# Kernel optimization log

Hardware: AMD Instinct MI355X
Metric: run time of the kernel (lower is better)

The kernel has to match this reference:

```python
import jax, jax.numpy as jnp
import numpy as np

B, CIN, H, W = 16, 3, 256, 256
COUT = 64
K = 3          # kernel size
PAD = 1
KK = K * K     # 9 taps
EPS = 1e-5     # BatchNorm eps


def conv3x3(x, w, b=None):
    y = jax.lax.conv_general_dilated(
        x, w, window_strides=(1, 1), padding=[(PAD, PAD), (PAD, PAD)],
        dimension_numbers=("NCHW", "OIHW", "NCHW"))
    if b is not None:
        y = y + b[None, :, None, None]
    return y


def deform_sample(x, off):
    """Bilinear sampling at per-pixel learned offsets (mmcv DeformConv2d, deform_groups=1).
    x: [B,C,H,W], off: [B,2*KK,H,W] interleaved (dy,dx) per kernel tap.
    Returns sampled taps [B,KK,H,W,C]."""
    b, c, h, w = x.shape
    dy = off[:, 0::2]  # [B,KK,H,W]
    dx = off[:, 1::2]
    ky, kx = jnp.meshgrid(jnp.arange(K), jnp.arange(K), indexing="ij")
    ky = (ky.reshape(-1) - PAD).astype(x.dtype)  # tap row offsets: -1,0,1
    kx = (kx.reshape(-1) - PAD).astype(x.dtype)
    gy = jnp.arange(h, dtype=x.dtype)
    gx = jnp.arange(w, dtype=x.dtype)
    # absolute (float) sampling positions per tap
    py = gy[None, None, :, None] + ky[None, :, None, None] + dy  # [B,KK,H,W]
    px = gx[None, None, None, :] + kx[None, :, None, None] + dx
    y0 = jnp.floor(py)
    x0 = jnp.floor(px)
    ly = py - y0
    lx = px - x0
    hy = 1.0 - ly
    hx = 1.0 - lx
    xt = x.transpose(0, 2, 3, 1)  # [B,H,W,C] for channel-last gather
    bi = jnp.arange(b)[:, None, None, None]

    def corner(yi, xi, wgt):
        valid = ((yi >= 0) & (yi <= h - 1) & (xi >= 0) & (xi <= w - 1)).astype(x.dtype)
        yc = jnp.clip(yi, 0, h - 1).astype(jnp.int32)
        xc = jnp.clip(xi, 0, w - 1).astype(jnp.int32)
        return xt[bi, yc, xc] * (wgt * valid)[..., None]  # [B,KK,H,W,C]

    v = (corner(y0, x0, hy * hx)
         + corner(y0, x0 + 1.0, hy * lx)
         + corner(y0 + 1.0, x0, ly * hx)
         + corner(y0 + 1.0, x0 + 1.0, ly * lx))
    return v


def setup_inputs() -> dict:
    key = jax.random.key(0)
    ks = jax.random.split(key, 7)
    x = jax.random.normal(ks[0], (B, CIN, H, W), dtype=jnp.float32)
    # conv_offset: 3x3 conv -> 2*KK offset channels (zero-init in mmcv; use small random)
    w_off = jax.random.normal(ks[1], (2 * KK, CIN, K, K), dtype=jnp.float32) * 0.01
    b_off = jnp.zeros((2 * KK,), dtype=jnp.float32)
    fan = CIN * KK
    w_dcn = jax.random.normal(ks[2], (COUT, CIN, K, K), dtype=jnp.float32) / np.sqrt(fan)
    w_conv = jax.random.normal(ks[3], (COUT, CIN, K, K), dtype=jnp.float32) / np.sqrt(fan)
    b_conv = jax.random.normal(ks[4], (COUT,), dtype=jnp.float32) * 0.01
    gamma = jnp.ones((COUT,), dtype=jnp.float32)
    beta = jnp.zeros((COUT,), dtype=jnp.float32)
    return {"x": x, "w_off": w_off, "b_off": b_off, "w_dcn": w_dcn,
            "w_conv": w_conv, "b_conv": b_conv, "gamma": gamma, "beta": beta}


def reference(x, w_off, b_off, w_dcn, w_conv, b_conv, gamma, beta):
    off = conv3x3(x, w_off, b_off)              # [B,18,H,W]
    taps = deform_sample(x, off)                # [B,KK,H,W,CIN]
    wk = w_dcn.reshape(COUT, CIN, KK).transpose(0, 2, 1)  # [O,KK,C]
    x_dcn = jnp.einsum("bkhwc,okc->bohw", taps, wk)       # deform conv (bias=False)
    x_res = conv3x3(x, w_conv, b_conv)
    y = x_res + x_dcn
    # BatchNorm2d (training mode: batch statistics, biased var)
    mean = y.mean(axis=(0, 2, 3))
    var = y.var(axis=(0, 2, 3))
    yn = (y - mean[None, :, None, None]) * jax.lax.rsqrt(var[None, :, None, None] + EPS)
    yb = yn * gamma[None, :, None, None] + beta[None, :, None, None]
    return yb * jax.nn.sigmoid(yb)  # SiLU
```

## Files before the change

kernel.cpp:

```cpp
#include <hip/hip_runtime.h>
#include <hip/hip_bf16.h>
#include <math.h>

#define BB 16
#define COUTC 64
#define HH 256
#define WWD 256
#define PW 260
#define NBLK (BB*HH)
#define NBLKW (NBLK*4)
#define NPIX (BB*HH*WWD)
#define YTOT ((size_t)NPIX*COUTC)

typedef __attribute__((ext_vector_type(8))) short short8;
typedef __attribute__((ext_vector_type(4))) float f32x4;
typedef __attribute__((ext_vector_type(4))) unsigned short us4;
typedef __attribute__((ext_vector_type(8))) unsigned short us8;

__device__ __forceinline__ unsigned short f2bf(float f) {
    __hip_bfloat16 h = __float2bfloat16(f);
    return __builtin_bit_cast(unsigned short, h);
}
__device__ __forceinline__ float bf2f(unsigned short u) {
    unsigned v = (unsigned)u << 16;
    return __builtin_bit_cast(float, v);
}

__global__ __launch_bounds__(256) void prep_kernel(
    const float* __restrict__ x,
    us4* __restrict__ xp)
{
    const int b  = blockIdx.x / PW;
    const int yr = blockIdx.x % PW - 2;
    const bool rok = (yr >= 0) && (yr < HH);
    const float* xb = x + (size_t)b * (3*HH*WWD) + (size_t)(rok ? yr : 0)*WWD;
    for (int cx = threadIdx.x; cx < PW; cx += 256) {
        const int xx = cx - 2;
        const bool ok = rok && (xx >= 0) && (xx < WWD);
        float f0 = ok ? xb[0*(HH*WWD) + xx] : 0.f;
        float f1 = ok ? xb[1*(HH*WWD) + xx] : 0.f;
        float f2 = ok ? xb[2*(HH*WWD) + xx] : 0.f;
        us4 v = { f2bf(f0), f2bf(f1), f2bf(f2), 0 };
        xp[((size_t)b*PW + (yr+2))*PW + cx] = v;
    }
}

__global__ __launch_bounds__(256) void wtg_kernel(
    const float* __restrict__ w_dcn,
    const float* __restrict__ w_conv,
    const float* __restrict__ w_off,
    unsigned short* __restrict__ wTg,
    unsigned short* __restrict__ wOg)
{
    for (int e = threadIdx.x; e < 512; e += 256) {
        const int kc = e >> 6, n = e & 63;
        const float* wsrc = (kc < 4) ? w_conv : w_dcn;
        const int kb = (kc & 3) * 8;
        us8 v;
        #pragma unroll
        for (int j = 0; j < 8; ++j) {
            int kk = kb + j;
            v[j] = (kk < 27) ? f2bf(wsrc[n*27 + kk]) : (unsigned short)0;
        }
        *(us8*)(wTg + e*8) = v;
    }
    if (threadIdx.x < 128) {
        const int e = threadIdx.x;
        const int nt2 = e >> 6, l = e & 63;
        const int n = nt2*16 + (l & 15);
        const int kb = (l >> 4) * 8;
        us8 v;
        #pragma unroll
        for (int j = 0; j < 8; ++j) {
            int kk = kb + j;
            v[j] = (n < 18 && kk < 27) ? f2bf(w_off[n*27 + kk]) : (unsigned short)0;
        }
        *(us8*)(wOg + e*8) = v;
    }
}

template<bool BF16Y>
__global__ __launch_bounds__(256, 3) void dcn_wave_kernel(
    const float* __restrict__ x,
    const us4* __restrict__ xp,
    const unsigned short* __restrict__ wTg,
    const unsigned short* __restrict__ wOg,
    const float* __restrict__ b_off,
    const float* __restrict__ b_conv,
    float* __restrict__ outf,
    unsigned short* __restrict__ yws,
    float* __restrict__ psum,
    float* __restrict__ psq)
{
    __shared__ __align__(16) char kbuf[32768];
    __shared__ __align__(16) unsigned short sofs[4*64*24];

    const int tid = threadIdx.x;
    const int bid = blockIdx.x;
    const int swz = (bid & 7) * 512 + (bid >> 3);
    const int b = swz >> 8;
    const int h = swz & 255;
    const int w = tid;
    const int l   = tid & 63;
    const int wv  = tid >> 6;
    const int g   = l >> 4;
    const int r15 = l & 15;
    char* kw = kbuf + wv*8192;
    unsigned short* so = sofs + wv*64*24;

    const us4* xpb = xp + (size_t)b*PW*PW;

    us4 xnv[3][3];
    #pragma unroll
    for (int dy = 0; dy < 3; ++dy)
        #pragma unroll
        for (int dx = 0; dx < 3; ++dx)
            xnv[dy][dx] = xpb[(size_t)(h+1+dy)*PW + (w+1+dx)];

    short8 bfr[2][4];
    #pragma unroll
    for (int ks = 0; ks < 2; ++ks)
        #pragma unroll
        for (int nt = 0; nt < 4; ++nt) {
            const int kc = ks*4 + g, n = nt*16 + r15;
            bfr[ks][nt] = *(const short8*)(wTg + (kc*64 + n)*8);
        }
    short8 wof[2];
    #pragma unroll
    for (int nt2 = 0; nt2 < 2; ++nt2)
        wof[nt2] = *(const short8*)(wOg + (nt2*64 + l)*8);

    {
        unsigned short u[32];
        #pragma unroll
        for (int c = 0; c < 3; ++c)
            #pragma unroll
            for (int ky = 0; ky < 3; ++ky)
                #pragma unroll
                for (int kx = 0; kx < 3; ++kx)
                    u[c*9 + ky*3 + kx] = xnv[ky][kx][c];
        #pragma unroll
        for (int k = 27; k < 32; ++k) u[k] = 0;
        #pragma unroll
        for (int c8 = 0; c8 < 4; ++c8) {
            uint4 v;
            v.x = (unsigned)u[c8*8+0] | ((unsigned)u[c8*8+1] << 16);
            v.y = (unsigned)u[c8*8+2] | ((unsigned)u[c8*8+3] << 16);
            v.z = (unsigned)u[c8*8+4] | ((unsigned)u[c8*8+5] << 16);
            v.w = (unsigned)u[c8*8+6] | ((unsigned)u[c8*8+7] << 16);
            *(uint4*)(kw + l*128 + ((c8 ^ (l & 7)) << 4)) = v;
        }
    }

    short8 af0[4];
    #pragma unroll
    for (int mt = 0; mt < 4; ++mt) {
        int row = mt*16 + r15;
        af0[mt] = *(const short8*)(kw + row*128 + ((g ^ (row & 7)) << 4));
    }

    f32x4 dacc[4][2];
    #pragma unroll
    for (int mt = 0; mt < 4; ++mt)
        #pragma unroll
        for (int nt2 = 0; nt2 < 2; ++nt2)
            dacc[mt][nt2] = (f32x4){0.f, 0.f, 0.f, 0.f};
    #pragma unroll
    for (int mt = 0; mt < 4; ++mt)
        #pragma unroll
        for (int nt2 = 0; nt2 < 2; ++nt2)
            dacc[mt][nt2] = __builtin_amdgcn_mfma_f32_16x16x32_bf16(
                af0[mt], wof[nt2], dacc[mt][nt2], 0, 0, 0);

    #pragma unroll
    for (int mt = 0; mt < 4; ++mt)
        #pragma unroll
        for (int nt2 = 0; nt2 < 2; ++nt2) {
            if (nt2 == 1 && r15 >= 2) continue;
            #pragma unroll
            for (int r = 0; r < 4; ++r)
                so[(mt*16 + g*4 + r)*24 + nt2*16 + r15] = f2bf(dacc[mt][nt2][r]);
        }

    float off[18];
    {
        us8 o0 = *(const us8*)(so + l*24);
        us8 o1 = *(const us8*)(so + l*24 + 8);
        us4 o2 = *(const us4*)(so + l*24 + 16);
        #pragma unroll
        for (int j = 0; j < 8; ++j)  off[j]     = bf2f(o0[j]) + b_off[j];
        #pragma unroll
        for (int j = 0; j < 8; ++j)  off[8+j]   = bf2f(o1[j]) + b_off[8+j];
        off[16] = bf2f(o2[0]) + b_off[16];
        off[17] = bf2f(o2[1]) + b_off[17];
    }

    float taps[9][3];
    #pragma unroll
    for (int k = 0; k < 9; ++k) {
        const int ky = k / 3, kx = k % 3;
        float py = (float)(h + ky - 1) + off[2*k];
        float px = (float)(w + kx - 1) + off[2*k + 1];
        float y0f = floorf(py), x0f = floorf(px);
        float ly = py - y0f, lx = px - x0f;
        float hy = 1.f - ly, hx = 1.f - lx;
        int y0 = (int)y0f, x0 = (int)x0f;

        if (__builtin_expect(y0 >= -2 && y0 <= 256 && x0 >= -2 && x0 <= 256, 1)) {
            const us4* p0 = xpb + (size_t)(y0+2)*PW + (x0+2);
            us4 c00 = p0[0],   c01 = p0[1];
            us4 c10 = p0[PW],  c11 = p0[PW+1];
            float w00 = hy*hx, w01 = hy*lx, w10 = ly*hx, w11 = ly*lx;
            #pragma unroll
            for (int c = 0; c < 3; ++c)
                taps[k][c] = w00*bf2f(c00[c]) + w01*bf2f(c01[c])
                           + w10*bf2f(c10[c]) + w11*bf2f(c11[c]);
        } else {
            int y1 = y0 + 1, x1 = x0 + 1;
            bool vy0 = (y0 >= 0) && (y0 < HH);
            bool vy1 = (y1 >= 0) && (y1 < HH);
            bool vx0 = (x0 >= 0) && (x0 < WWD);
            bool vx1 = (x1 >= 0) && (x1 < WWD);
            float w00 = (vy0 && vx0) ? hy*hx : 0.f;
            float w01 = (vy0 && vx1) ? hy*lx : 0.f;
            float w10 = (vy1 && vx0) ? ly*hx : 0.f;
            float w11 = (vy1 && vx1) ? ly*lx : 0.f;
            int yc0 = min(max(y0, 0), HH-1),  yc1 = min(max(y1, 0), HH-1);
            int xc0 = min(max(x0, 0), WWD-1), xc1 = min(max(x1, 0), WWD-1);
            const float* xb = x + (size_t)b * (3*HH*WWD);
            #pragma unroll
            for (int c = 0; c < 3; ++c) {
                const float* xc = xb + c*(HH*WWD);
                taps[k][c] = w00*xc[yc0*WWD+xc0] + w01*xc[yc0*WWD+xc1]
                           + w10*xc[yc1*WWD+xc0] + w11*xc[yc1*WWD+xc1];
            }
        }
    }

    {
        unsigned short u[32];
        #pragma unroll
        for (int c = 0; c < 3; ++c)
            #pragma unroll
            for (int kt = 0; kt < 9; ++kt)
                u[c*9 + kt] = f2bf(taps[kt][c]);
        #pragma unroll
        for (int k = 27; k < 32; ++k) u[k] = 0;
        #pragma unroll
        for (int c8 = 4; c8 < 8; ++c8) {
            const int j0 = (c8 - 4) * 8;
            uint4 v;
            v.x = (unsigned)u[j0+0] | ((unsigned)u[j0+1] << 16);
            v.y = (unsigned)u[j0+2] | ((unsigned)u[j0+3] << 16);
            v.z = (unsigned)u[j0+4] | ((unsigned)u[j0+5] << 16);
            v.w = (unsigned)u[j0+6] | ((unsigned)u[j0+7] << 16);
            *(uint4*)(kw + l*128 + ((c8 ^ (l & 7)) << 4)) = v;
        }
    }

    short8 a1[4];
    #pragma unroll
    for (int mt = 0; mt < 4; ++mt) {
        int row = mt*16 + r15;
        int chunk = 4 + g;
        a1[mt] = *(const short8*)(kw + row*128 + ((chunk ^ (row & 7)) << 4));
    }

    #pragma unroll
    for (int nt = 0; nt < 4; ++nt) {
        f32x4 acc[4];
        #pragma unroll
        for (int mt = 0; mt < 4; ++mt)
            acc[mt] = (f32x4){0.f, 0.f, 0.f, 0.f};
        #pragma unroll
        for (int mt = 0; mt < 4; ++mt)
            acc[mt] = __builtin_amdgcn_mfma_f32_16x16x32_bf16(af0[mt], bfr[0][nt], acc[mt], 0, 0, 0);
        #pragma unroll
        for (int mt = 0; mt < 4; ++mt)
            acc[mt] = __builtin_amdgcn_mfma_f32_16x16x32_bf16(a1[mt],  bfr[1][nt], acc[mt], 0, 0, 0);

        const float bcv = b_conv[nt*16 + r15];
        float s = 0.f, s2 = 0.f;
        const size_t base = ((size_t)(b*64 + nt*16 + r15) << 16)
                          + (size_t)h*256 + wv*64 + g*4;
        #pragma unroll
        for (int mt = 0; mt < 4; ++mt) {
            f32x4 v = acc[mt];
            float ox = v.x + bcv, oy = v.y + bcv, oz = v.z + bcv, ow = v.w + bcv;
            s += ox + oy + oz + ow;
            s2 = fmaf(ox, ox, s2); s2 = fmaf(oy, oy, s2);
            s2 = fmaf(oz, oz, s2); s2 = fmaf(ow, ow, s2);
            if (BF16Y) {
                us4 pv = { f2bf(ox), f2bf(oy), f2bf(oz), f2bf(ow) };
                *(us4*)(yws + base + mt*16) = pv;
            } else {
                float4 pv = { ox, oy, oz, ow };
                *(float4*)(outf + base + mt*16) = pv;
            }
        }
        s  += __shfl_xor(s, 16);  s  += __shfl_xor(s, 32);
        s2 += __shfl_xor(s2, 16); s2 += __shfl_xor(s2, 32);
        if (l < 16) {
            psum[(nt*16 + l)*NBLKW + swz*4 + wv] = s;
            psq [(nt*16 + l)*NBLKW + swz*4 + wv] = s2;
        }
    }
}

__global__ __launch_bounds__(256) void bn_stats_kernel(
    const float* __restrict__ psum,
    const float* __restrict__ psq,
    const float* __restrict__ gamma,
    const float* __restrict__ beta,
    float* __restrict__ ss)
{
    __shared__ float rs[256], rq[256];
    const int ch = blockIdx.x, tid = threadIdx.x;
    float s = 0.f, s2 = 0.f;
    for (int j = tid; j < NBLKW; j += 256) {
        s  += psum[ch*NBLKW + j];
        s2 += psq [ch*NBLKW + j];
    }
    rs[tid] = s; rq[tid] = s2;
    __syncthreads();
    for (int st = 128; st > 0; st >>= 1) {
        if (tid < st) { rs[tid] += rs[tid + st]; rq[tid] += rq[tid + st]; }
        __syncthreads();
    }
    if (tid == 0) {
        const float N = (float)NPIX;
        float mean = rs[0] / N;
        float var  = rq[0] / N - mean*mean;
        float rstd = rsqrtf(var + 1e-5f);
        float sc   = gamma[ch] * rstd;
        ss[ch]      = sc;
        ss[64 + ch] = beta[ch] - mean * sc;
    }
}

__global__ __launch_bounds__(256) void bn_silu_bf16_kernel(
    const unsigned short* __restrict__ yws,
    float* __restrict__ out,
    const float* __restrict__ ss)
{
    __shared__ float sc[64], sh[64];
    if (threadIdx.x < 64) {
        sc[threadIdx.x] = ss[threadIdx.x];
        sh[threadIdx.x] = ss[64 + threadIdx.x];
    }
    __syncthreads();
    const int total8 = (int)(YTOT / 8);
    for (int i = blockIdx.x*256 + threadIdx.x; i < total8; i += gridDim.x*256) {
        us8 v = *(const us8*)(yws + (size_t)i*8);
        const int o = (i >> 13) & 63;
        const float a = sc[o], t = sh[o];
        float e[8];
        #pragma unroll
        for (int j = 0; j < 8; ++j) {
            float z = fmaf(bf2f(v[j]), a, t);
            e[j] = z / (1.f + __expf(-z));
        }
        float4 r0 = { e[0], e[1], e[2], e[3] };
        float4 r1 = { e[4], e[5], e[6], e[7] };
        *(float4*)(out + (size_t)i*8)     = r0;
        *(float4*)(out + (size_t)i*8 + 4) = r1;
    }
}

__global__ __launch_bounds__(256) void bn_silu_kernel(
    float* __restrict__ y,
    const float* __restrict__ ss)
{
    __shared__ float sc[64], sh[64];
    if (threadIdx.x < 64) {
        sc[threadIdx.x] = ss[threadIdx.x];
        sh[threadIdx.x] = ss[64 + threadIdx.x];
    }
    __syncthreads();
    float4* y4 = (float4*)y;
    const int total4 = (int)(YTOT / 4);
    for (int i = blockIdx.x*256 + threadIdx.x; i < total4; i += gridDim.x*256) {
        float4 v = y4[i];
        const int o = (i >> 14) & 63;
        const float a = sc[o], t = sh[o];
        float z;
        z = fmaf(v.x, a, t); v.x = z / (1.f + __expf(-z));
        z = fmaf(v.y, a, t); v.y = z / (1.f + __expf(-z));
        z = fmaf(v.z, a, t); v.z = z / (1.f + __expf(-z));
        z = fmaf(v.w, a, t); v.w = z / (1.f + __expf(-z));
        y4[i] = v;
    }
}

extern "C" void kernel_launch(void* const* d_in, const int* in_sizes, int n_in,
                              void* d_out, int out_size, void* d_ws, size_t ws_size,
                              hipStream_t stream) {
    const float* x      = (const float*)d_in[0];
    const float* w_off  = (const float*)d_in[1];
    const float* b_off  = (const float*)d_in[2];
    const float* w_dcn  = (const float*)d_in[3];
    const float* w_conv = (const float*)d_in[4];
    const float* b_conv = (const float*)d_in[5];
    const float* gamma  = (const float*)d_in[6];
    const float* beta   = (const float*)d_in[7];
    float* out = (float*)d_out;

    const size_t yBytes    = YTOT * 2;
    const size_t xpBytes   = (size_t)BB*PW*PW*8;
    const size_t wtgBytes  = 8192 + 2048;
    const size_t statBytes = 2*(size_t)64*NBLKW*4 + 512;

    if (ws_size >= yBytes + xpBytes + wtgBytes + statBytes) {
        unsigned short* yws = (unsigned short*)d_ws;
        us4*            xpp = (us4*)((char*)d_ws + yBytes);
        unsigned short* wTg = (unsigned short*)((char*)d_ws + yBytes + xpBytes);
        unsigned short* wOg = wTg + 4096;
        float* psum = (float*)((char*)d_ws + yBytes + xpBytes + wtgBytes);
        float* psq  = psum + (size_t)64*NBLKW;
        float* ss   = psq  + (size_t)64*NBLKW;
        prep_kernel<<<BB*PW, 256, 0, stream>>>(x, xpp);
        wtg_kernel<<<1, 256, 0, stream>>>(w_dcn, w_conv, w_off, wTg, wOg);
        dcn_wave_kernel<true><<<NBLK, 256, 0, stream>>>(
            x, xpp, wTg, wOg, b_off, b_conv, nullptr, yws, psum, psq);
        bn_stats_kernel<<<64, 256, 0, stream>>>(psum, psq, gamma, beta, ss);
        bn_silu_bf16_kernel<<<2048, 256, 0, stream>>>(yws, out, ss);
    } else {
        us4*            xpp = (us4*)d_ws;
        unsigned short* wTg = (unsigned short*)((char*)d_ws + xpBytes);
        unsigned short* wOg = wTg + 4096;
        float* psum = (float*)((char*)d_ws + xpBytes + wtgBytes);
        float* psq  = psum + (size_t)64*NBLKW;
        float* ss   = psq  + (size_t)64*NBLKW;
        prep_kernel<<<BB*PW, 256, 0, stream>>>(x, xpp);
        wtg_kernel<<<1, 256, 0, stream>>>(w_dcn, w_conv, w_off, wTg, wOg);
        dcn_wave_kernel<false><<<NBLK, 256, 0, stream>>>(
            x, xpp, wTg, wOg, b_off, b_conv, out, nullptr, psum, psq);
        bn_stats_kernel<<<64, 256, 0, stream>>>(psum, psq, gamma, beta, ss);
        bn_silu_kernel<<<2048, 256, 0, stream>>>(out, ss);
    }
}
```

Measured before the change: 186.2 us.

## Process two rows per block with prefetch of next row's neighborhood

The DCN kernel now launches half as many blocks, and each block handles two image rows in sequence. The next row's 3x3 input neighborhood is loaded early, between the offset-conv MFMA and the bilinear sampling, so its latency overlaps with work on the current row. Neighborhood and bilinear corner loads are also widened to 16-byte us8 reads in place of several us4 reads. In exchange the kernel holds more registers and exposes less block-level parallelism.

```diff
diff --git a/kernel.cpp b/kernel.cpp
--- a/kernel.cpp
+++ b/kernel.cpp
@@ -8,6 +8,7 @@
 #define WWD 256
 #define PW 260
 #define NBLK (BB*HH)
+#define NBLK2 2048
 #define NBLKW (NBLK*4)
 #define NPIX (BB*HH*WWD)
 #define YTOT ((size_t)NPIX*COUTC)
@@ -79,6 +80,17 @@
     }
 }
 
+__device__ __forceinline__ void load_xn3(const us4* __restrict__ xpb, int h, int w,
+                                         us8 r8[3], us4 r4[3])
+{
+    #pragma unroll
+    for (int dy = 0; dy < 3; ++dy) {
+        const us4* p = xpb + (size_t)(h+1+dy)*PW + (w+1);
+        r8[dy] = *(const us8*)p;
+        r4[dy] = p[2];
+    }
+}
+
 template<bool BF16Y>
 __global__ __launch_bounds__(256, 3) void dcn_wave_kernel(
     const float* __restrict__ x,
@@ -97,9 +109,6 @@
 
     const int tid = threadIdx.x;
     const int bid = blockIdx.x;
-    const int swz = (bid & 7) * 512 + (bid >> 3);
-    const int b = swz >> 8;
-    const int h = swz & 255;
     const int w = tid;
     const int l   = tid & 63;
     const int wv  = tid >> 6;
@@ -108,15 +117,6 @@
     char* kw = kbuf + wv*8192;
     unsigned short* so = sofs + wv*64*24;
 
-    const us4* xpb = xp + (size_t)b*PW*PW;
-
-    us4 xnv[3][3];
-    #pragma unroll
-    for (int dy = 0; dy < 3; ++dy)
-        #pragma unroll
-        for (int dx = 0; dx < 3; ++dx)
-            xnv[dy][dx] = xpb[(size_t)(h+1+dy)*PW + (w+1+dx)];
-
     short8 bfr[2][4];
     #pragma unroll
     for (int ks = 0; ks < 2; ++ks)
@@ -130,179 +130,200 @@
     for (int nt2 = 0; nt2 < 2; ++nt2)
         wof[nt2] = *(const short8*)(wOg + (nt2*64 + l)*8);
 
-    {
-        unsigned short u[32];
-        #pragma unroll
-        for (int c = 0; c < 3; ++c)
-            #pragma unroll
-            for (int ky = 0; ky < 3; ++ky)
+    int eff = bid;
+    int swz = ((eff & 7) << 9) | (eff >> 3);
+    int b = swz >> 8, h = swz & 255;
+    const us4* xpb = xp + (size_t)b*PW*PW;
+    us8 c8v[3]; us4 c4v[3];
+    load_xn3(xpb, h, w, c8v, c4v);
+
+    #pragma unroll
+    for (int it = 0; it < 2; ++it) {
+        const int eff_n = eff + NBLK2;
+        const int swz_n = ((eff_n & 7) << 9) | ((eff_n >> 3) & 511);
+        const int b_n = swz_n >> 8, h_n = swz_n & 255;
+        const us4* xpb_n = xp + (size_t)b_n*PW*PW;
+
+        {
+            unsigned short u[32];
+            #pragma unroll
+            for (int c = 0; c < 3; ++c)
                 #pragma unroll
-                for (int kx = 0; kx < 3; ++kx)
-                    u[c*9 + ky*3 + kx] = xnv[ky][kx][c];
-        #pragma unroll
-        for (int k = 27; k < 32; ++k) u[k] = 0;
-        #pragma unroll
-        for (int c8 = 0; c8 < 4; ++c8) {
-            uint4 v;
-            v.x = (unsigned)u[c8*8+0] | ((unsigned)u[c8*8+1] << 16);
-            v.y = (unsigned)u[c8*8+2] | ((unsigned)u[c8*8+3] << 16);
-            v.z = (unsigned)u[c8*8+4] | ((unsigned)u[c8*8+5] << 16);
-            v.w = (unsigned)u[c8*8+6] | ((unsigned)u[c8*8+7] << 16);
-            *(uint4*)(kw + l*128 + ((c8 ^ (l & 7)) << 4)) = v;
-        }
-    }
-
-    short8 af0[4];
-    #pragma unroll
-    for (int mt = 0; mt < 4; ++mt) {
-        int row = mt*16 + r15;
-        af0[mt] = *(const short8*)(kw + row*128 + ((g ^ (row & 7)) << 4));
-    }
-
-    f32x4 dacc[4][2];
-    #pragma unroll
-    for (int mt = 0; mt < 4; ++mt)
-        #pragma unroll
-        for (int nt2 = 0; nt2 < 2; ++nt2)
-            dacc[mt][nt2] = (f32x4){0.f, 0.f, 0.f, 0.f};
-    #pragma unroll
-    for (int mt = 0; mt < 4; ++mt)
-        #pragma unroll
-        for (int nt2 = 0; nt2 < 2; ++nt2)
-            dacc[mt][nt2] = __builtin_amdgcn_mfma_f32_16x16x32_bf16(
-                af0[mt], wof[nt2], dacc[mt][nt2], 0, 0, 0);
-
-    #pragma unroll
-    for (int mt = 0; mt < 4; ++mt)
-        #pragma unroll
-        for (int nt2 = 0; nt2 < 2; ++nt2) {
-            if (nt2 == 1 && r15 >= 2) continue;
-            #pragma unroll
-            for (int r = 0; r < 4; ++r)
-                so[(mt*16 + g*4 + r)*24 + nt2*16 + r15] = f2bf(dacc[mt][nt2][r]);
-        }
-
-    float off[18];
-    {
-        us8 o0 = *(const us8*)(so + l*24);
-        us8 o1 = *(const us8*)(so + l*24 + 8);
-        us4 o2 = *(const us4*)(so + l*24 + 16);
-        #pragma unroll
-        for (int j = 0; j < 8; ++j)  off[j]     = bf2f(o0[j]) + b_off[j];
-        #pragma unroll
-        for (int j = 0; j < 8; ++j)  off[8+j]   = bf2f(o1[j]) + b_off[8+j];
-        off[16] = bf2f(o2[0]) + b_off[16];
-        off[17] = bf2f(o2[1]) + b_off[17];
-    }
-
-    float taps[9][3];
-    #pragma unroll
-    for (int k = 0; k < 9; ++k) {
-        const int ky = k / 3, kx = k % 3;
-        float py = (float)(h + ky - 1) + off[2*k];
-        float px = (float)(w + kx - 1) + off[2*k + 1];
-        float y0f = floorf(py), x0f = floorf(px);
-        float ly = py - y0f, lx = px - x0f;
-        float hy = 1.f - ly, hx = 1.f - lx;
-        int y0 = (int)y0f, x0 = (int)x0f;
-
-        if (__builtin_expect(y0 >= -2 && y0 <= 256 && x0 >= -2 && x0 <= 256, 1)) {
-            const us4* p0 = xpb + (size_t)(y0+2)*PW + (x0+2);
-            us4 c00 = p0[0],   c01 = p0[1];
-            us4 c10 = p0[PW],  c11 = p0[PW+1];
-            float w00 = hy*hx, w01 = hy*lx, w10 = ly*hx, w11 = ly*lx;
-            #pragma unroll
-            for (int c = 0; c < 3; ++c)
-                taps[k][c] = w00*bf2f(c00[c]) + w01*bf2f(c01[c])
-                           + w10*bf2f(c10[c]) + w11*bf2f(c11[c]);
-        } else {
-            int y1 = y0 + 1, x1 = x0 + 1;
-            bool vy0 = (y0 >= 0) && (y0 < HH);
-            bool vy1 = (y1 >= 0) && (y1 < HH);
-            bool vx0 = (x0 >= 0) && (x0 < WWD);
-            bool vx1 = (x1 >= 0) && (x1 < WWD);
-            float w00 = (vy0 && vx0) ? hy*hx : 0.f;
-            float w01 = (vy0 && vx1) ? hy*lx : 0.f;
-            float w10 = (vy1 && vx0) ? ly*hx : 0.f;
-            float w11 = (vy1 && vx1) ? ly*lx : 0.f;
-            int yc0 = min(max(y0, 0), HH-1),  yc1 = min(max(y1, 0), HH-1);
-            int xc0 = min(max(x0, 0), WWD-1), xc1 = min(max(x1, 0), WWD-1);
-            const float* xb = x + (size_t)b * (3*HH*WWD);
-            #pragma unroll
-            for (int c = 0; c < 3; ++c) {
-                const float* xc = xb + c*(HH*WWD);
-                taps[k][c] = w00*xc[yc0*WWD+xc0] + w01*xc[yc0*WWD+xc1]
-                           + w10*xc[yc1*WWD+xc0] + w11*xc[yc1*WWD+xc1];
-            }
-        }
-    }
-
-    {
-        unsigned short u[32];
-        #pragma unroll
-        for (int c = 0; c < 3; ++c)
-            #pragma unroll
-            for (int kt = 0; kt < 9; ++kt)
-                u[c*9 + kt] = f2bf(taps[kt][c]);
-        #pragma unroll
-        for (int k = 27; k < 32; ++k) u[k] = 0;
+                for (int ky = 0; ky < 3; ++ky)
+                    #pragma unroll
+                    for (int kx = 0; kx < 3; ++kx)
+                        u[c*9 + ky*3 + kx] = (kx == 2) ? c4v[ky][c]
+                                                       : c8v[ky][kx*4 + c];
+            #pragma unroll
+            for (int k = 27; k < 32; ++k) u[k] = 0;
+            #pragma unroll
+            for (int c8 = 0; c8 < 4; ++c8) {
+                uint4 v;
+                v.x = (unsigned)u[c8*8+0] | ((unsigned)u[c8*8+1] << 16);
+                v.y = (unsigned)u[c8*8+2] | ((unsigned)u[c8*8+3] << 16);
+                v.z = (unsigned)u[c8*8+4] | ((unsigned)u[c8*8+5] << 16);
+                v.w = (unsigned)u[c8*8+6] | ((unsigned)u[c8*8+7] << 16);
+                *(uint4*)(kw + l*128 + ((c8 ^ (l & 7)) << 4)) = v;
+            }
+        }
+
+        f32x4 dacc[4][2];
+        {
+            short8 af0[4];
+            #pragma unroll
+            for (int mt = 0; mt < 4; ++mt) {
+                int row = mt*16 + r15;
+                af0[mt] = *(const short8*)(kw + row*128 + ((g ^ (row & 7)) << 4));
+            }
+            #pragma unroll
+            for (int mt = 0; mt < 4; ++mt)
+                #pragma unroll
+                for (int nt2 = 0; nt2 < 2; ++nt2) {
+                    dacc[mt][nt2] = (f32x4){0.f, 0.f, 0.f, 0.f};
+                    dacc[mt][nt2] = __builtin_amdgcn_mfma_f32_16x16x32_bf16(
+                        af0[mt], wof[nt2], dacc[mt][nt2], 0, 0, 0);
+                }
+        }
+
+        #pragma unroll
+        for (int mt = 0; mt < 4; ++mt)
+            #pragma unroll
+            for (int nt2 = 0; nt2 < 2; ++nt2) {
+                if (nt2 == 1 && r15 >= 2) continue;
+                #pragma unroll
+                for (int r = 0; r < 4; ++r)
+                    so[(mt*16 + g*4 + r)*24 + nt2*16 + r15] = f2bf(dacc[mt][nt2][r]);
+            }
+
+        us8 n8[3]; us4 n4[3];
+        if (it == 0) load_xn3(xpb_n, h_n, w, n8, n4);
+
+        float off[18];
+        {
+            us8 o0 = *(const us8*)(so + l*24);
+            us8 o1 = *(const us8*)(so + l*24 + 8);
+            us4 o2 = *(const us4*)(so + l*24 + 16);
+            #pragma unroll
+            for (int j = 0; j < 8; ++j)  off[j]   = bf2f(o0[j]) + b_off[j];
+            #pragma unroll
+            for (int j = 0; j < 8; ++j)  off[8+j] = bf2f(o1[j]) + b_off[8+j];
+            off[16] = bf2f(o2[0]) + b_off[16];
+            off[17] = bf2f(o2[1]) + b_off[17];
+        }
+
+        unsigned short ut[32];
+        #pragma unroll
+        for (int k = 0; k < 9; ++k) {
+            const int ky = k / 3, kx = k % 3;
+            float py = (float)(h + ky - 1) + off[2*k];
+            float px = (float)(w + kx - 1) + off[2*k + 1];
+            float y0f = floorf(py), x0f = floorf(px);
+            float ly = py - y0f, lx = px - x0f;
+            float hy = 1.f - ly, hx = 1.f - lx;
+            int y0 = (int)y0f, x0 = (int)x0f;
+            float t0, t1, t2;
+
+            if (__builtin_expect(y0 >= -2 && y0 <= 256 && x0 >= -2 && x0 <= 256, 1)) {
+                const us4* p0 = xpb + (size_t)(y0+2)*PW + (x0+2);
+                us8 r0 = *(const us8*)p0;
+                us8 r1 = *(const us8*)(p0 + PW);
+                float w00 = hy*hx, w01 = hy*lx, w10 = ly*hx, w11 = ly*lx;
+                t0 = w00*bf2f(r0[0]) + w01*bf2f(r0[4]) + w10*bf2f(r1[0]) + w11*bf2f(r1[4]);
+                t1 = w00*bf2f(r0[1]) + w01*bf2f(r0[5]) + w10*bf2f(r1[1]) + w11*bf2f(r1[5]);
+                t2 = w00*bf2f(r0[2]) + w01*bf2f(r0[6]) + w10*bf2f(r1[2]) + w11*bf2f(r1[6]);
+            } else {
+                int y1 = y0 + 1, x1 = x0 + 1;
+                bool vy0 = (y0 >= 0) && (y0 < HH);
+                bool vy1 = (y1 >= 0) && (y1 < HH);
+                bool vx0 = (x0 >= 0) && (x0 < WWD);
+                bool vx1 = (x1 >= 0) && (x1 < WWD);
+                float w00 = (vy0 && vx0) ? hy*hx : 0.f;
+                float w01 = (vy0 && vx1) ? hy*lx : 0.f;
+                float w10 = (vy1 && vx0) ? ly*hx : 0.f;
+                float w11 = (vy1 && vx1) ? ly*lx : 0.f;
+                int yc0 = min(max(y0, 0), HH-1),  yc1 = min(max(y1, 0), HH-1);
+                int xc0 = min(max(x0, 0), WWD-1), xc1 = min(max(x1, 0), WWD-1);
+                const float* xb = x + (size_t)b * (3*HH*WWD);
+                const float* x0p = xb;
+                t0 = w00*x0p[yc0*WWD+xc0] + w01*x0p[yc0*WWD+xc1]
+                   + w10*x0p[yc1*WWD+xc0] + w11*x0p[yc1*WWD+xc1];
+                const float* x1p = xb + HH*WWD;
+                t1 = w00*x1p[yc0*WWD+xc0] + w01*x1p[yc0*WWD+xc1]
+                   + w10*x1p[yc1*WWD+xc0] + w11*x1p[yc1*WWD+xc1];
+                const float* x2p = xb + 2*HH*WWD;
+                t2 = w00*x2p[yc0*WWD+xc0] + w01*x2p[yc0*WWD+xc1]
+                   + w10*x2p[yc1*WWD+xc0] + w11*x2p[yc1*WWD+xc1];
+            }
+            ut[0*9 + k] = f2bf(t0);
+            ut[1*9 + k] = f2bf(t1);
+            ut[2*9 + k] = f2bf(t2);
+        }
+        #pragma unroll
+        for (int k = 27; k < 32; ++k) ut[k] = 0;
+
         #pragma unroll
         for (int c8 = 4; c8 < 8; ++c8) {
             const int j0 = (c8 - 4) * 8;
             uint4 v;
-            v.x = (unsigned)u[j0+0] | ((unsigned)u[j0+1] << 16);
-            v.y = (unsigned)u[j0+2] | ((unsigned)u[j0+3] << 16);
-            v.z = (unsigned)u[j0+4] | ((unsigned)u[j0+5] << 16);
-            v.w = (unsigned)u[j0+6] | ((unsigned)u[j0+7] << 16);
+            v.x = (unsigned)ut[j0+0] | ((unsigned)ut[j0+1] << 16);
+            v.y = (unsigned)ut[j0+2] | ((unsigned)ut[j0+3] << 16);
+            v.z = (unsigned)ut[j0+4] | ((unsigned)ut[j0+5] << 16);
+            v.w = (unsigned)ut[j0+6] | ((unsigned)ut[j0+7] << 16);
             *(uint4*)(kw + l*128 + ((c8 ^ (l & 7)) << 4)) = v;
         }
-    }
-
-    short8 a1[4];
-    #pragma unroll
-    for (int mt = 0; mt < 4; ++mt) {
-        int row = mt*16 + r15;
-        int chunk = 4 + g;
-        a1[mt] = *(const short8*)(kw + row*128 + ((chunk ^ (row & 7)) << 4));
-    }
-
-    #pragma unroll
-    for (int nt = 0; nt < 4; ++nt) {
-        f32x4 acc[4];
-        #pragma unroll
-        for (int mt = 0; mt < 4; ++mt)
-            acc[mt] = (f32x4){0.f, 0.f, 0.f, 0.f};
-        #pragma unroll
-        for (int mt = 0; mt < 4; ++mt)
-            acc[mt] = __builtin_amdgcn_mfma_f32_16x16x32_bf16(af0[mt], bfr[0][nt], acc[mt], 0, 0, 0);
-        #pragma unroll
-        for (int mt = 0; mt < 4; ++mt)
-            acc[mt] = __builtin_amdgcn_mfma_f32_16x16x32_bf16(a1[mt],  bfr[1][nt], acc[mt], 0, 0, 0);
-
-        const float bcv = b_conv[nt*16 + r15];
-        float s = 0.f, s2 = 0.f;
-        const size_t base = ((size_t)(b*64 + nt*16 + r15) << 16)
-                          + (size_t)h*256 + wv*64 + g*4;
+
+        short8 a0[4], a1[4];
         #pragma unroll
         for (int mt = 0; mt < 4; ++mt) {
-            f32x4 v = acc[mt];
-            float ox = v.x + bcv, oy = v.y + bcv, oz = v.z + bcv, ow = v.w + bcv;
-            s += ox + oy + oz + ow;
-            s2 = fmaf(ox, ox, s2); s2 = fmaf(oy, oy, s2);
-            s2 = fmaf(oz, oz, s2); s2 = fmaf(ow, ow, s2);
-            if (BF16Y) {
-                us4 pv = { f2bf(ox), f2bf(oy), f2bf(oz), f2bf(ow) };
-                *(us4*)(yws + base + mt*16) = pv;
-            } else {
-                float4 pv = { ox, oy, oz, ow };
-                *(float4*)(outf + base + mt*16) = pv;
-            }
-        }
-        s  += __shfl_xor(s, 16);  s  += __shfl_xor(s, 32);
-        s2 += __shfl_xor(s2, 16); s2 += __shfl_xor(s2, 32);
-        if (l < 16) {
-            psum[(nt*16 + l)*NBLKW + swz*4 + wv] = s;
-            psq [(nt*16 + l)*NBLKW + swz*4 + wv] = s2;
+            int row = mt*16 + r15;
+            a0[mt] = *(const short8*)(kw + row*128 + (( g      ^ (row & 7)) << 4));
+            a1[mt] = *(const short8*)(kw + row*128 + (((4 + g) ^ (row & 7)) << 4));
+        }
+
+        #pragma unroll
+        for (int nt = 0; nt < 4; ++nt) {
+            f32x4 acc[4];
+            #pragma unroll
+            for (int mt = 0; mt < 4; ++mt)
+                acc[mt] = (f32x4){0.f, 0.f, 0.f, 0.f};
+            #pragma unroll
+            for (int mt = 0; mt < 4; ++mt)
+                acc[mt] = __builtin_amdgcn_mfma_f32_16x16x32_bf16(a0[mt], bfr[0][nt], acc[mt], 0, 0, 0);
+            #pragma unroll
+            for (int mt = 0; mt < 4; ++mt)
+                acc[mt] = __builtin_amdgcn_mfma_f32_16x16x32_bf16(a1[mt], bfr[1][nt], acc[mt], 0, 0, 0);
+
+            const float bcv = b_conv[nt*16 + r15];
+            float s = 0.f, s2 = 0.f;
+            const size_t base = ((size_t)(b*64 + nt*16 + r15) << 16)
+                              + (size_t)h*256 + wv*64 + g*4;
+            #pragma unroll
+            for (int mt = 0; mt < 4; ++mt) {
+                f32x4 v = acc[mt];
+                float ox = v.x + bcv, oy = v.y + bcv, oz = v.z + bcv, ow = v.w + bcv;
+                s += ox + oy + oz + ow;
+                s2 = fmaf(ox, ox, s2); s2 = fmaf(oy, oy, s2);
+                s2 = fmaf(oz, oz, s2); s2 = fmaf(ow, ow, s2);
+                if (BF16Y) {
+                    us4 pv = { f2bf(ox), f2bf(oy), f2bf(oz), f2bf(ow) };
+                    *(us4*)(yws + base + mt*16) = pv;
+                } else {
+                    float4 pv = { ox, oy, oz, ow };
+                    *(float4*)(outf + base + mt*16) = pv;
+                }
+            }
+            s  += __shfl_xor(s, 16);  s  += __shfl_xor(s, 32);
+            s2 += __shfl_xor(s2, 16); s2 += __shfl_xor(s2, 32);
+            if (l < 16) {
+                psum[(nt*16 + l)*NBLKW + swz*4 + wv] = s;
+                psq [(nt*16 + l)*NBLKW + swz*4 + wv] = s2;
+            }
+        }
+
+        if (it == 0) {
+            eff = eff_n; swz = swz_n; b = b_n; h = h_n; xpb = xpb_n;
+            #pragma unroll
+            for (int dy = 0; dy < 3; ++dy) { c8v[dy] = n8[dy]; c4v[dy] = n4[dy]; }
         }
     }
 }
@@ -420,7 +441,7 @@
         float* ss   = psq  + (size_t)64*NBLKW;
         prep_kernel<<<BB*PW, 256, 0, stream>>>(x, xpp);
         wtg_kernel<<<1, 256, 0, stream>>>(w_dcn, w_conv, w_off, wTg, wOg);
-        dcn_wave_kernel<true><<<NBLK, 256, 0, stream>>>(
+        dcn_wave_kernel<true><<<NBLK2, 256, 0, stream>>>(
             x, xpp, wTg, wOg, b_off, b_conv, nullptr, yws, psum, psq);
         bn_stats_kernel<<<64, 256, 0, stream>>>(psum, psq, gamma, beta, ss);
         bn_silu_bf16_kernel<<<2048, 256, 0, stream>>>(yws, out, ss);
@@ -433,7 +454,7 @@
         float* ss   = psq  + (size_t)64*NBLKW;
         prep_kernel<<<BB*PW, 256, 0, stream>>>(x, xpp);
         wtg_kernel<<<1, 256, 0, stream>>>(w_dcn, w_conv, w_off, wTg, wOg);
-        dcn_wave_kernel<false><<<NBLK, 256, 0, stream>>>(
+        dcn_wave_kernel<false><<<NBLK2, 256, 0, stream>>>(
             x, xpp, wTg, wOg, b_off, b_conv, out, nullptr, psum, psq);
         bn_stats_kernel<<<64, 256, 0, stream>>>(psum, psq, gamma, beta, ss);
         bn_silu_kernel<<<2048, 256, 0, stream>>>(out, ss);
```

Measured after the change: 184.8 us. No clear change (-0.8%).
